# Performance work log

Measured on AMD Instinct MI355X. Metric: run time of the kernel, lower is better.

The kernel has to match this reference:

```python
import jax, jax.numpy as jnp
import numpy as np

B, N, C, D, H = 2, 1024, 64, 512, 16
HD = D // H
LENGTH_SCALE = 0.22
LN_EPS = 1e-5


def _ln(x, g, b):
    m = jnp.mean(x, axis=-1, keepdims=True)
    v = jnp.var(x, axis=-1, keepdims=True)
    return g * (x - m) * jax.lax.rsqrt(v + LN_EPS) + b


def _distance_affinity(positions, length_scale):
    # Gaussian affinity in [0,1]: exp(-||pi - pj||^2 / (2 ls^2))
    d2 = jnp.sum((positions[:, :, None, :] - positions[:, None, :, :]) ** 2, axis=-1)
    return jnp.exp(-d2 / (2.0 * length_scale * length_scale))


def setup_inputs() -> dict:
    key = jax.random.key(0)
    ks = jax.random.split(key, 24)
    p = lambda k, s: (jax.random.normal(k, s) * 0.02).astype(jnp.float32)
    hidden = jax.random.normal(ks[0], (B, N, D), jnp.float32)
    adjacency = (jax.random.uniform(ks[1], (B, N, N)) < 0.05).astype(jnp.float32)
    positions = jax.random.uniform(ks[2], (B, N, 2), jnp.float32)
    context_tokens = jax.random.normal(ks[3], (B, C, D), jnp.float32)
    edge_head_conditioning = (jax.random.normal(ks[4], (B, 4, N, N)) * 0.1).astype(jnp.float32)
    return {
        'hidden': hidden, 'adjacency': adjacency, 'positions': positions,
        'context_tokens': context_tokens, 'edge_head_conditioning': edge_head_conditioning,
        'Wq': p(ks[5], (D, D)), 'bq': jnp.zeros((D,), jnp.float32),
        'Wk': p(ks[6], (D, D)), 'bk': jnp.zeros((D,), jnp.float32),
        'Wv': p(ks[7], (D, D)), 'bv': jnp.zeros((D,), jnp.float32),
        'Wo': p(ks[8], (D, D)), 'bo': jnp.zeros((D,), jnp.float32),
        'ln1_g': jnp.ones((D,), jnp.float32), 'ln1_b': jnp.zeros((D,), jnp.float32),
        'ln2_g': jnp.ones((D,), jnp.float32), 'ln2_b': jnp.zeros((D,), jnp.float32),
        'W1': p(ks[9], (4 * D, D)), 'b1': jnp.zeros((4 * D,), jnp.float32),
        'W2': p(ks[10], (D, 4 * D)), 'b2': jnp.zeros((D,), jnp.float32),
    }


def _forward(hidden, adjacency, positions, context_tokens, edge_head_conditioning,
             Wq, bq, Wk, bk, Wv, bv, Wo, bo, ln1_g, ln1_b, ln2_g, ln2_b, W1, b1, W2, b2):
    b, n, d = hidden.shape
    cc = context_tokens.shape[1]
    hd = d // H
    n1 = _ln(hidden, ln1_g, ln1_b)
    nc = _ln(context_tokens, ln1_g, ln1_b)
    key_source = jnp.concatenate([n1, nc], axis=1)          # [b, m, d]
    m = n + cc
    q = (n1 @ Wq.T + bq).reshape(b, n, H, hd).transpose(0, 2, 1, 3)          # [b,h,n,hd]
    k = (key_source @ Wk.T + bk).reshape(b, m, H, hd).transpose(0, 2, 1, 3)  # [b,h,m,hd]
    v = (key_source @ Wv.T + bv).reshape(b, m, H, hd).transpose(0, 2, 1, 3)
    logits = jnp.einsum('bhnd,bhmd->bhnm', q, k) / jnp.sqrt(jnp.float32(hd))

    pad = jnp.zeros((b, n, cc), logits.dtype)
    dist_e = jnp.concatenate([_distance_affinity(positions, LENGTH_SCALE), pad], axis=-1)  # [b,n,m]
    adj_e = jnp.concatenate([adjacency, pad], axis=-1)                                      # [b,n,m]
    edge_e = jnp.concatenate([edge_head_conditioning,
                              jnp.zeros((b, 4, n, cc), logits.dtype)], axis=-1)             # [b,4,n,m]

    # heads 0:4 distance, 4:8 connectivity, 8:12 stress (edge cond), 12:16 free
    bias = jnp.concatenate([
        jnp.broadcast_to((2.0 * dist_e - 1.0)[:, None], (b, 4, n, m)),
        jnp.broadcast_to((2.0 * adj_e - 1.0)[:, None], (b, 4, n, m)),
        edge_e,
        jnp.zeros((b, 4, n, m), logits.dtype)], axis=1)
    scale = jnp.concatenate([
        jnp.broadcast_to((0.25 + 0.75 * dist_e)[:, None], (b, 4, n, m)),
        jnp.broadcast_to((0.25 + 0.75 * adj_e)[:, None], (b, 4, n, m)),
        jnp.ones((b, 8, n, m), logits.dtype)], axis=1)

    w = jax.nn.softmax(logits + bias, axis=-1) * scale
    w = w / jnp.maximum(jnp.sum(w, axis=-1, keepdims=True), 1e-6)
    att = jnp.einsum('bhnm,bhmd->bhnd', w, v).transpose(0, 2, 1, 3).reshape(b, n, d)
    hidden = hidden + att @ Wo.T + bo
    n2 = _ln(hidden, ln2_g, ln2_b)
    ff = jax.nn.gelu(n2 @ W1.T + b1, approximate=False) @ W2.T + b2
    return hidden + ff


def reference(hidden, adjacency, positions, context_tokens, edge_head_conditioning,
              Wq, bq, Wk, bk, Wv, bv, Wo, bo, ln1_g, ln1_b, ln2_g, ln2_b, W1, b1, W2, b2):
    return _forward(hidden, adjacency, positions, context_tokens, edge_head_conditioning,
                    Wq, bq, Wk, bk, Wv, bv, Wo, bo, ln1_g, ln1_b, ln2_g, ln2_b, W1, b1, W2, b2)
```

## Files before the change

### kernel.cpp

```cpp
#include <hip/hip_runtime.h>
#include <math.h>

typedef unsigned short u16;
typedef unsigned int u32;
typedef __attribute__((ext_vector_type(8))) short short8;
typedef __attribute__((ext_vector_type(8))) u16 ushort8_t;
typedef __attribute__((ext_vector_type(4))) u16 ushort4_t;
typedef __attribute__((ext_vector_type(4))) float floatx4;

#define DEV static __device__ __forceinline__

DEV u16 f2b(float f) {
    union { float f; u32 u; } v; v.f = f;
    u32 u = v.u;
    return (u16)((u + 0x7fffu + ((u >> 16) & 1u)) >> 16);
}
DEV float gelu_f(float x) {
    return 0.5f * x * (1.f + erff(x * 0.70710678118654752f));
}

__global__ __launch_bounds__(256) void cvt_weights(
    const float* __restrict__ wq, const float* __restrict__ wk,
    const float* __restrict__ wv, const float* __restrict__ wo,
    const float* __restrict__ w1, const float* __restrict__ w2,
    u16* __restrict__ oq, u16* __restrict__ ok, u16* __restrict__ ov,
    u16* __restrict__ oo, u16* __restrict__ o1, u16* __restrict__ o2)
{
    long i = ((long)blockIdx.x * 256 + threadIdx.x) * 4;
    const float* s; u16* d; long off;
    if (i < 1048576) {
        int seg = (int)(i >> 18);
        off = i & 262143;
        s = seg == 0 ? wq : seg == 1 ? wk : seg == 2 ? wv : wo;
        d = seg == 0 ? oq : seg == 1 ? ok : seg == 2 ? ov : oo;
    } else if (i < 2097152) {
        off = i - 1048576; s = w1; d = o1;
    } else {
        off = i - 2097152; s = w2; d = o2;
    }
    floatx4 v = *(const floatx4*)(s + off);
    ushort4_t r;
    r[0] = f2b(v[0]); r[1] = f2b(v[1]); r[2] = f2b(v[2]); r[3] = f2b(v[3]);
    *(ushort4_t*)(d + off) = r;
}

__global__ __launch_bounds__(256) void ln_kernel(
    const float* __restrict__ hidden, const float* __restrict__ ctx,
    const float* __restrict__ g, const float* __restrict__ bta,
    u16* __restrict__ dst, int nrows)
{
    int wid = threadIdx.x >> 6, lane = threadIdx.x & 63;
    int row = blockIdx.x * 4 + wid;
    if (row >= nrows) return;
    int bi = row / 1088, loc = row % 1088;
    const float* src = (loc < 1024) ? hidden + ((long)(bi * 1024 + loc)) * 512
                                    : ctx + ((long)(bi * 64 + (loc - 1024))) * 512;
    const floatx4* p = (const floatx4*)(src + lane * 8);
    floatx4 a = p[0], b4 = p[1];
    float x[8];
    x[0] = a[0]; x[1] = a[1]; x[2] = a[2]; x[3] = a[3];
    x[4] = b4[0]; x[5] = b4[1]; x[6] = b4[2]; x[7] = b4[3];
    float s = 0.f, sq = 0.f;
#pragma unroll
    for (int j = 0; j < 8; j++) { s += x[j]; sq += x[j] * x[j]; }
#pragma unroll
    for (int m = 1; m < 64; m <<= 1) {
        s += __shfl_xor(s, m, 64);
        sq += __shfl_xor(sq, m, 64);
    }
    float mean = s * (1.f / 512.f);
    float var = sq * (1.f / 512.f) - mean * mean;
    float rstd = rsqrtf(var + 1e-5f);
    const floatx4* gp = (const floatx4*)(g + lane * 8);
    const floatx4* bp = (const floatx4*)(bta + lane * 8);
    floatx4 g0 = gp[0], g1 = gp[1], bb0 = bp[0], bb1 = bp[1];
    float gg[8], bbv[8];
    gg[0] = g0[0]; gg[1] = g0[1]; gg[2] = g0[2]; gg[3] = g0[3];
    gg[4] = g1[0]; gg[5] = g1[1]; gg[6] = g1[2]; gg[7] = g1[3];
    bbv[0] = bb0[0]; bbv[1] = bb0[1]; bbv[2] = bb0[2]; bbv[3] = bb0[3];
    bbv[4] = bb1[0]; bbv[5] = bb1[1]; bbv[6] = bb1[2]; bbv[7] = bb1[3];
    ushort8_t o;
#pragma unroll
    for (int j = 0; j < 8; j++) o[j] = f2b((x[j] - mean) * rstd * gg[j] + bbv[j]);
    *(ushort8_t*)(dst + (long)row * 512 + lane * 8) = o;
}

template<int ACT, int OMODE>
__global__ __launch_bounds__(256) void gemm_bt(
    const u16* __restrict__ A, const u16* __restrict__ Bw,
    const float* __restrict__ bias0, const float* __restrict__ bias1,
    const float* __restrict__ bias2,
    float* __restrict__ outf, u16* __restrict__ outb0,
    u16* __restrict__ outb1, u16* __restrict__ outb2,
    int M, int N, int K, int ksp)
{
    __shared__ u16 As[128 * 72];
    __shared__ u16 Bs[128 * 72];
    int tid = threadIdx.x;
    int wid = tid >> 6, lane = tid & 63;
    int l16 = lane & 15, lq = lane >> 4;
    int m0 = blockIdx.y * 128, n0 = blockIdx.x * 128;
    int wm = (wid >> 1) * 64, wn = (wid & 1) * 64;
    int srow = tid >> 3;
    int scol = (tid & 7) * 8;
    int kb0 = (OMODE == 4) ? blockIdx.z * ksp : 0;
    int kend = (OMODE == 4) ? kb0 + ksp : K;
    floatx4 acc[4][4] = {};
    for (int k0 = kb0; k0 < kend; k0 += 64) {
#pragma unroll
        for (int p = 0; p < 4; p++) {
            int r = p * 32 + srow;
            *(ushort8_t*)(As + r * 72 + scol) =
                *(const ushort8_t*)(A + (long)(m0 + r) * K + k0 + scol);
            *(ushort8_t*)(Bs + r * 72 + scol) =
                *(const ushort8_t*)(Bw + (long)(n0 + r) * K + k0 + scol);
        }
        __syncthreads();
#pragma unroll
        for (int s = 0; s < 2; s++) {
            short8 af[4], bfr[4];
#pragma unroll
            for (int i = 0; i < 4; i++)
                af[i] = *(const short8*)(As + (wm + i * 16 + l16) * 72 + s * 32 + lq * 8);
#pragma unroll
            for (int j = 0; j < 4; j++)
                bfr[j] = *(const short8*)(Bs + (wn + j * 16 + l16) * 72 + s * 32 + lq * 8);
#pragma unroll
            for (int i = 0; i < 4; i++)
#pragma unroll
                for (int j = 0; j < 4; j++)
                    acc[i][j] = __builtin_amdgcn_mfma_f32_16x16x32_bf16(
                        af[i], bfr[j], acc[i][j], 0, 0, 0);
        }
        __syncthreads();
    }
#pragma unroll
    for (int i = 0; i < 4; i++) {
#pragma unroll
        for (int j = 0; j < 4; j++) {
            int gmb = m0 + wm + i * 16 + lq * 4;
            int gn = n0 + wn + j * 16 + l16;
#pragma unroll
            for (int r = 0; r < 4; r++) {
                int gm = gmb + r;
                float v = acc[i][j][r];
                if (OMODE == 1) {
                    v += bias0[gn];
                    if (ACT == 1) v = gelu_f(v);
                    outb0[(long)gm * N + gn] = f2b(v);
                } else if (OMODE == 3) {
                    if (gn < 512) {
                        outb0[(long)gm * 512 + gn] = f2b(v + bias0[gn]);
                    } else if (gn < 1024) {
                        outb1[(long)gm * 512 + gn - 512] = f2b(v + bias1[gn - 512]);
                    } else {
                        int bi = gm / 1088, tok = gm % 1088;
                        int col = gn - 1024;
                        outb2[((long)((bi * 16 + (col >> 5)) * 32 + (col & 31))) * 1088 + tok]
                            = f2b(v + bias2[col]);
                    }
                } else {
                    outf[((long)blockIdx.z * M + gm) * N + gn] = v;
                }
            }
        }
    }
}

__global__ __launch_bounds__(256) void attn_kernel(
    const u16* __restrict__ qb, const u16* __restrict__ kb,
    const u16* __restrict__ vt, const float* __restrict__ adj,
    const float* __restrict__ pos, const float* __restrict__ ehc,
    float* __restrict__ o_part, float* __restrict__ l_part)
{
    __shared__ u16 P[4][16 * 72];
    __shared__ float ubuf[4][1088];
    int b = blockIdx.z >> 1, split = blockIdx.z & 1;
    int h = blockIdx.y, grp = h >> 2;
    int qbase = blockIdx.x * 64;
    int tid = threadIdx.x, wid = tid >> 6, lane = tid & 63;
    int l16 = lane & 15, lq = lane >> 4;
    int kv_begin = split ? 576 : 0;
    int kv_end = split ? 1088 : 576;
    const float inv2ls2 = 10.330578512396695f;
    const float rs = 0.17677669529663687f;
    float* pls = &ubuf[0][0];
    float* bt = ubuf[wid];

    if (grp == 0) {
        for (int t = tid; t < 2048; t += 256) pls[t] = pos[b * 2048 + t];
        __syncthreads();
    }
    int rowbase = qbase + wid * 16;
    int qrow = rowbase + l16;
    short8 qa = *(const short8*)(qb + ((long)(b * 1088 + qrow)) * 512 + h * 32 + lq * 8);
    int irow[4];
#pragma unroll
    for (int r = 0; r < 4; r++) irow[r] = rowbase + lq * 4 + r;
    float ipx[4], ipy[4];
    if (grp == 0) {
#pragma unroll
        for (int r = 0; r < 4; r++) {
            ipx[r] = pls[irow[r] * 2];
            ipy[r] = pls[irow[r] * 2 + 1];
        }
    }

    bool stg = (grp == 1 || grp == 2);
    const float* src = (grp == 1)
        ? adj + ((long)(b * 1024 + rowbase)) * 1024
        : ehc + (((long)(b * 4 + (h - 8))) * 1024 + rowbase) * 1024;
    int row4 = lane >> 4, c16 = (lane & 15) * 4;
    floatx4 pre[4];

    float rsum[4] = {0.f, 0.f, 0.f, 0.f};
    floatx4 o[2] = {};
    floatx4 zacc = {0.f, 0.f, 0.f, 0.f};
    u16* Pw = P[wid];

    if (stg && kv_begin < 1024) {
#pragma unroll
        for (int p = 0; p < 4; p++)
            pre[p] = *(const floatx4*)(src + (long)(p * 4 + row4) * 1024 + kv_begin + c16);
#pragma unroll
        for (int p = 0; p < 4; p++)
            *(floatx4*)(bt + (p * 4 + row4) * 68 + c16) = pre[p];
    }

    for (int kv = kv_begin; kv < kv_end; kv += 64) {
        floatx4 sfr[4];
#pragma unroll
        for (int jf = 0; jf < 4; jf++) {
            int tok = kv + jf * 16 + l16;
            short8 kf = *(const short8*)(kb + ((long)(b * 1088 + tok)) * 512 + h * 32 + lq * 8);
            sfr[jf] = __builtin_amdgcn_mfma_f32_16x16x32_bf16(qa, kf, zacc, 0, 0, 0);
        }
        int kvn = kv + 64;
        bool pf = stg && kvn < kv_end && kvn < 1024;
        if (pf) {
#pragma unroll
            for (int p = 0; p < 4; p++)
                pre[p] = *(const floatx4*)(src + (long)(p * 4 + row4) * 1024 + kvn + c16);
        }
#pragma unroll
        for (int jf = 0; jf < 4; jf++) {
            int j = kv + jf * 16 + l16;
            float px = 0.f, py = 0.f;
            if (grp == 0 && j < 1024) { px = pls[2 * j]; py = pls[2 * j + 1]; }
#pragma unroll
            for (int r = 0; r < 4; r++) {
                float bias, scale;
                if (grp == 0) {
                    if (j < 1024) {
                        float dx = ipx[r] - px, dy = ipy[r] - py;
                        float e = __expf(-(dx * dx + dy * dy) * inv2ls2);
                        bias = 2.f * e - 1.f; scale = 0.25f + 0.75f * e;
                    } else { bias = -1.f; scale = 0.25f; }
                } else if (grp == 1) {
                    if (j < 1024) {
                        float a = bt[(lq * 4 + r) * 68 + jf * 16 + l16];
                        bias = 2.f * a - 1.f; scale = 0.25f + 0.75f * a;
                    } else { bias = -1.f; scale = 0.25f; }
                } else if (grp == 2) {
                    bias = (j < 1024) ? bt[(lq * 4 + r) * 68 + jf * 16 + l16] : 0.f;
                    scale = 1.f;
                } else { bias = 0.f; scale = 1.f; }
                float sv = fminf(sfr[jf][r] * rs + bias, 60.f);
                float p = __expf(sv) * scale;
                rsum[r] += p;
                Pw[(lq * 4 + r) * 72 + jf * 16 + l16] = f2b(p);
            }
        }
#pragma unroll
        for (int s = 0; s < 2; s++) {
            short8 pa = *(const short8*)(Pw + l16 * 72 + s * 32 + lq * 8);
#pragma unroll
            for (int nf = 0; nf < 2; nf++) {
                const u16* vrow = vt + ((long)((b * 16 + h) * 32 + nf * 16 + l16)) * 1088
                                  + kv + s * 32 + lq * 8;
                short8 vf = *(const short8*)vrow;
                o[nf] = __builtin_amdgcn_mfma_f32_16x16x32_bf16(pa, vf, o[nf], 0, 0, 0);
            }
        }
        if (pf) {
#pragma unroll
            for (int p = 0; p < 4; p++)
                *(floatx4*)(bt + (p * 4 + row4) * 68 + c16) = pre[p];
        }
    }
#pragma unroll
    for (int r = 0; r < 4; r++) {
#pragma unroll
        for (int m = 1; m < 16; m <<= 1)
            rsum[r] += __shfl_xor(rsum[r], m, 64);
    }
    long pb = (((long)(split * 2 + b) * 16 + h) * 1024);
#pragma unroll
    for (int nf = 0; nf < 2; nf++)
#pragma unroll
        for (int r = 0; r < 4; r++)
            o_part[(pb + irow[r]) * 32 + nf * 16 + l16] = o[nf][r];
    if (l16 == 0) {
#pragma unroll
        for (int r = 0; r < 4; r++) l_part[pb + irow[r]] = rsum[r];
    }
}

__global__ __launch_bounds__(256) void attn_combine(
    const float* __restrict__ o_part, const float* __restrict__ l_part,
    u16* __restrict__ att)
{
    int idx = blockIdx.x * 256 + threadIdx.x;
    int c4 = idx & 7;
    int row = (idx >> 3) & 1023;
    int h = (idx >> 13) & 15;
    int b = (idx >> 17) & 1;
    long base = (((long)b * 16 + h) * 1024 + row) * 32 + c4 * 4;
    floatx4 a0 = *(const floatx4*)(o_part + base);
    floatx4 a1 = *(const floatx4*)(o_part + 1048576 + base);
    long lb0 = ((long)b * 16 + h) * 1024 + row;
    float inv = 1.f / (l_part[lb0] + l_part[32768 + lb0]);
    ushort4_t w;
#pragma unroll
    for (int e = 0; e < 4; e++) w[e] = f2b((a0[e] + a1[e]) * inv);
    *(ushort4_t*)(att + ((long)b * 1024 + row) * 512 + h * 32 + c4 * 4) = w;
}

__global__ __launch_bounds__(256) void wo_ln2(
    const float* __restrict__ p0, const float* __restrict__ p1,
    const float* __restrict__ bo, const float* __restrict__ hidden,
    const float* __restrict__ g, const float* __restrict__ bta,
    float* __restrict__ h2, u16* __restrict__ n2)
{
    int wid = threadIdx.x >> 6, lane = threadIdx.x & 63;
    int row = blockIdx.x * 4 + wid;
    long base = (long)row * 512 + lane * 8;
    float x[8];
#pragma unroll
    for (int hp = 0; hp < 2; hp++) {
        floatx4 a = *(const floatx4*)(hidden + base + hp * 4);
        floatx4 q0 = *(const floatx4*)(p0 + base + hp * 4);
        floatx4 q1 = *(const floatx4*)(p1 + base + hp * 4);
        floatx4 bb = *(const floatx4*)(bo + lane * 8 + hp * 4);
#pragma unroll
        for (int e = 0; e < 4; e++) x[hp * 4 + e] = a[e] + q0[e] + q1[e] + bb[e];
    }
    float s = 0.f, sq = 0.f;
#pragma unroll
    for (int j = 0; j < 8; j++) { s += x[j]; sq += x[j] * x[j]; }
#pragma unroll
    for (int m = 1; m < 64; m <<= 1) {
        s += __shfl_xor(s, m, 64);
        sq += __shfl_xor(sq, m, 64);
    }
    float mean = s * (1.f / 512.f);
    float var = sq * (1.f / 512.f) - mean * mean;
    float rstd = rsqrtf(var + 1e-5f);
#pragma unroll
    for (int hp = 0; hp < 2; hp++) {
        floatx4 w;
#pragma unroll
        for (int e = 0; e < 4; e++) w[e] = x[hp * 4 + e];
        *(floatx4*)(h2 + base + hp * 4) = w;
    }
    const floatx4* gp = (const floatx4*)(g + lane * 8);
    const floatx4* bp = (const floatx4*)(bta + lane * 8);
    floatx4 g0 = gp[0], g1 = gp[1], bb0 = bp[0], bb1 = bp[1];
    float gg[8], bbv[8];
    gg[0] = g0[0]; gg[1] = g0[1]; gg[2] = g0[2]; gg[3] = g0[3];
    gg[4] = g1[0]; gg[5] = g1[1]; gg[6] = g1[2]; gg[7] = g1[3];
    bbv[0] = bb0[0]; bbv[1] = bb0[1]; bbv[2] = bb0[2]; bbv[3] = bb0[3];
    bbv[4] = bb1[0]; bbv[5] = bb1[1]; bbv[6] = bb1[2]; bbv[7] = bb1[3];
    ushort8_t ov;
#pragma unroll
    for (int j = 0; j < 8; j++) ov[j] = f2b((x[j] - mean) * rstd * gg[j] + bbv[j]);
    *(ushort8_t*)(n2 + base) = ov;
}

__global__ __launch_bounds__(256) void ff2_ep(
    const float* __restrict__ parts, const float* __restrict__ b2,
    const float* __restrict__ h2, float* __restrict__ out)
{
    long idx = ((long)blockIdx.x * 256 + threadIdx.x) * 4;
    int col = (int)(idx & 511);
    floatx4 v = *(const floatx4*)(h2 + idx);
    floatx4 bb = *(const floatx4*)(b2 + col);
#pragma unroll
    for (int s = 0; s < 4; s++) {
        floatx4 p = *(const floatx4*)(parts + (long)s * 1048576 + idx);
#pragma unroll
        for (int e = 0; e < 4; e++) v[e] += p[e];
    }
#pragma unroll
    for (int e = 0; e < 4; e++) v[e] += bb[e];
    *(floatx4*)(out + idx) = v;
}

extern "C" void kernel_launch(void* const* d_in, const int* in_sizes, int n_in,
                              void* d_out, int out_size, void* d_ws, size_t ws_size,
                              hipStream_t stream) {
    const float* hidden = (const float*)d_in[0];
    const float* adjacency = (const float*)d_in[1];
    const float* positions = (const float*)d_in[2];
    const float* context = (const float*)d_in[3];
    const float* ehc = (const float*)d_in[4];
    const float* Wq = (const float*)d_in[5];
    const float* bq = (const float*)d_in[6];
    const float* Wk = (const float*)d_in[7];
    const float* bk = (const float*)d_in[8];
    const float* Wv = (const float*)d_in[9];
    const float* bv = (const float*)d_in[10];
    const float* Wo = (const float*)d_in[11];
    const float* bo = (const float*)d_in[12];
    const float* ln1g = (const float*)d_in[13];
    const float* ln1b = (const float*)d_in[14];
    const float* ln2g = (const float*)d_in[15];
    const float* ln2b = (const float*)d_in[16];
    const float* W1 = (const float*)d_in[17];
    const float* b1 = (const float*)d_in[18];
    const float* W2 = (const float*)d_in[19];
    const float* b2 = (const float*)d_in[20];
    float* out = (float*)d_out;

    char* ws = (char*)d_ws;
    u16* wqkv_b = (u16*)(ws + 0);
    u16* wo_b   = (u16*)(ws + 1572864);
    u16* w1_b   = (u16*)(ws + 2097152);
    u16* w2_b   = (u16*)(ws + 4194304);
    u16* ks_b   = (u16*)(ws + 6291456);
    u16* q_b    = (u16*)(ws + 8519680);
    u16* k_b    = (u16*)(ws + 10747904);
    u16* vt_b   = (u16*)(ws + 12976128);
    u16* att_b  = (u16*)(ws + 15204352);
    float* h2_f = (float*)(ws + 17301504);
    u16* n2_b   = (u16*)(ws + 21495808);
    u16* g_b    = (u16*)(ws + 23592960);
    float* o_part = (float*)(ws + 31981568);
    float* l_part = (float*)(ws + 40370176);
    float* wo_p  = (float*)(ws + 40632320);
    float* ff2_p = (float*)(ws + 49020928);

    cvt_weights<<<3072, 256, 0, stream>>>(Wq, Wk, Wv, Wo, W1, W2,
                                          wqkv_b, wqkv_b + 262144, wqkv_b + 524288,
                                          wo_b, w1_b, w2_b);
    ln_kernel<<<544, 256, 0, stream>>>(hidden, context, ln1g, ln1b, ks_b, 2176);
    gemm_bt<0, 3><<<dim3(12, 17), 256, 0, stream>>>(
        ks_b, wqkv_b, bq, bk, bv, nullptr, q_b, k_b, vt_b, 2176, 1536, 512, 0);
    attn_kernel<<<dim3(16, 16, 4), 256, 0, stream>>>(
        q_b, k_b, vt_b, adjacency, positions, ehc, o_part, l_part);
    attn_combine<<<1024, 256, 0, stream>>>(o_part, l_part, att_b);
    gemm_bt<0, 4><<<dim3(4, 16, 2), 256, 0, stream>>>(
        att_b, wo_b, nullptr, nullptr, nullptr, wo_p, nullptr, nullptr, nullptr,
        2048, 512, 512, 256);
    wo_ln2<<<512, 256, 0, stream>>>(wo_p, wo_p + 1048576, bo, hidden,
                                    ln2g, ln2b, h2_f, n2_b);
    gemm_bt<1, 1><<<dim3(16, 16), 256, 0, stream>>>(
        n2_b, w1_b, b1, nullptr, nullptr, nullptr, g_b, nullptr, nullptr,
        2048, 2048, 512, 0);
    gemm_bt<0, 4><<<dim3(4, 16, 4), 256, 0, stream>>>(
        g_b, w2_b, nullptr, nullptr, nullptr, ff2_p, nullptr, nullptr, nullptr,
        2048, 512, 2048, 512);
    ff2_ep<<<1024, 256, 0, stream>>>(ff2_p, b2, h2_f, out);
}
```

Before: 246.8 us.

## Fuse prep kernels, prefetch GEMM tiles, split attention four ways, atomic FF2 epilogue

Merges weight conversion and LN1 into one launch. The GEMM tile shrinks to 64x128 and next-tile global loads are register-prefetched behind the MFMA work. Attention KV is split four ways instead of two, the bias tile is stored in bf16 LDS, the q scaling is folded into the QKV epilogue, and the kernel gets an occupancy hint. The final FF2 GEMM atomically accumulates into the output, which wo_ln2 pre-initialises with residual plus b2, so the separate epilogue kernel is dropped. The cost is extra atomics and a bf16 rounding of the bias values.

```diff
diff --git a/kernel.cpp b/kernel.cpp
--- a/kernel.cpp
+++ b/kernel.cpp
@@ -15,43 +15,46 @@
     u32 u = v.u;
     return (u16)((u + 0x7fffu + ((u >> 16) & 1u)) >> 16);
 }
+DEV float b2f(u16 h) {
+    union { u32 u; float f; } v; v.u = ((u32)h) << 16;
+    return v.f;
+}
 DEV float gelu_f(float x) {
     return 0.5f * x * (1.f + erff(x * 0.70710678118654752f));
 }
 
-__global__ __launch_bounds__(256) void cvt_weights(
+__global__ __launch_bounds__(256) void cvt_ln(
     const float* __restrict__ wq, const float* __restrict__ wk,
     const float* __restrict__ wv, const float* __restrict__ wo,
     const float* __restrict__ w1, const float* __restrict__ w2,
     u16* __restrict__ oq, u16* __restrict__ ok, u16* __restrict__ ov,
-    u16* __restrict__ oo, u16* __restrict__ o1, u16* __restrict__ o2)
-{
-    long i = ((long)blockIdx.x * 256 + threadIdx.x) * 4;
-    const float* s; u16* d; long off;
-    if (i < 1048576) {
-        int seg = (int)(i >> 18);
-        off = i & 262143;
-        s = seg == 0 ? wq : seg == 1 ? wk : seg == 2 ? wv : wo;
-        d = seg == 0 ? oq : seg == 1 ? ok : seg == 2 ? ov : oo;
-    } else if (i < 2097152) {
-        off = i - 1048576; s = w1; d = o1;
-    } else {
-        off = i - 2097152; s = w2; d = o2;
-    }
-    floatx4 v = *(const floatx4*)(s + off);
-    ushort4_t r;
-    r[0] = f2b(v[0]); r[1] = f2b(v[1]); r[2] = f2b(v[2]); r[3] = f2b(v[3]);
-    *(ushort4_t*)(d + off) = r;
-}
-
-__global__ __launch_bounds__(256) void ln_kernel(
+    u16* __restrict__ oo, u16* __restrict__ o1, u16* __restrict__ o2,
     const float* __restrict__ hidden, const float* __restrict__ ctx,
     const float* __restrict__ g, const float* __restrict__ bta,
-    u16* __restrict__ dst, int nrows)
+    u16* __restrict__ dst)
 {
+    if (blockIdx.x < 3072) {
+        long i = ((long)blockIdx.x * 256 + threadIdx.x) * 4;
+        const float* s; u16* d; long off;
+        if (i < 1048576) {
+            int seg = (int)(i >> 18);
+            off = i & 262143;
+            s = seg == 0 ? wq : seg == 1 ? wk : seg == 2 ? wv : wo;
+            d = seg == 0 ? oq : seg == 1 ? ok : seg == 2 ? ov : oo;
+        } else if (i < 2097152) {
+            off = i - 1048576; s = w1; d = o1;
+        } else {
+            off = i - 2097152; s = w2; d = o2;
+        }
+        floatx4 v = *(const floatx4*)(s + off);
+        ushort4_t r;
+        r[0] = f2b(v[0]); r[1] = f2b(v[1]); r[2] = f2b(v[2]); r[3] = f2b(v[3]);
+        *(ushort4_t*)(d + off) = r;
+        return;
+    }
     int wid = threadIdx.x >> 6, lane = threadIdx.x & 63;
-    int row = blockIdx.x * 4 + wid;
-    if (row >= nrows) return;
+    int row = (blockIdx.x - 3072) * 4 + wid;
+    if (row >= 2176) return;
     int bi = row / 1088, loc = row % 1088;
     const float* src = (loc < 1024) ? hidden + ((long)(bi * 1024 + loc)) * 512
                                     : ctx + ((long)(bi * 64 + (loc - 1024))) * 512;
@@ -94,39 +97,55 @@
     u16* __restrict__ outb1, u16* __restrict__ outb2,
     int M, int N, int K, int ksp)
 {
-    __shared__ u16 As[128 * 72];
+    __shared__ u16 As[64 * 72];
     __shared__ u16 Bs[128 * 72];
     int tid = threadIdx.x;
     int wid = tid >> 6, lane = tid & 63;
     int l16 = lane & 15, lq = lane >> 4;
-    int m0 = blockIdx.y * 128, n0 = blockIdx.x * 128;
-    int wm = (wid >> 1) * 64, wn = (wid & 1) * 64;
+    int m0 = blockIdx.y * 64, n0 = blockIdx.x * 128;
+    int wm = (wid >> 1) * 32, wn = (wid & 1) * 64;
     int srow = tid >> 3;
     int scol = (tid & 7) * 8;
-    int kb0 = (OMODE == 4) ? blockIdx.z * ksp : 0;
-    int kend = (OMODE == 4) ? kb0 + ksp : K;
-    floatx4 acc[4][4] = {};
+    int kb0 = (OMODE >= 4) ? blockIdx.z * ksp : 0;
+    int kend = (OMODE >= 4) ? kb0 + ksp : K;
+    floatx4 acc[2][4] = {};
+    const u16* Ap = A + (long)(m0 + srow) * K + scol;
+    const u16* Bp = Bw + (long)(n0 + srow) * K + scol;
+    ushort8_t pa[2], pb[4];
+#pragma unroll
+    for (int p = 0; p < 2; p++)
+        pa[p] = *(const ushort8_t*)(Ap + (long)p * 32 * K + kb0);
+#pragma unroll
+    for (int p = 0; p < 4; p++)
+        pb[p] = *(const ushort8_t*)(Bp + (long)p * 32 * K + kb0);
     for (int k0 = kb0; k0 < kend; k0 += 64) {
 #pragma unroll
-        for (int p = 0; p < 4; p++) {
-            int r = p * 32 + srow;
-            *(ushort8_t*)(As + r * 72 + scol) =
-                *(const ushort8_t*)(A + (long)(m0 + r) * K + k0 + scol);
-            *(ushort8_t*)(Bs + r * 72 + scol) =
-                *(const ushort8_t*)(Bw + (long)(n0 + r) * K + k0 + scol);
-        }
+        for (int p = 0; p < 2; p++)
+            *(ushort8_t*)(As + (p * 32 + srow) * 72 + scol) = pa[p];
+#pragma unroll
+        for (int p = 0; p < 4; p++)
+            *(ushort8_t*)(Bs + (p * 32 + srow) * 72 + scol) = pb[p];
         __syncthreads();
+        int k1 = k0 + 64;
+        if (k1 < kend) {
+#pragma unroll
+            for (int p = 0; p < 2; p++)
+                pa[p] = *(const ushort8_t*)(Ap + (long)p * 32 * K + k1);
+#pragma unroll
+            for (int p = 0; p < 4; p++)
+                pb[p] = *(const ushort8_t*)(Bp + (long)p * 32 * K + k1);
+        }
 #pragma unroll
         for (int s = 0; s < 2; s++) {
-            short8 af[4], bfr[4];
-#pragma unroll
-            for (int i = 0; i < 4; i++)
+            short8 af[2], bfr[4];
+#pragma unroll
+            for (int i = 0; i < 2; i++)
                 af[i] = *(const short8*)(As + (wm + i * 16 + l16) * 72 + s * 32 + lq * 8);
 #pragma unroll
             for (int j = 0; j < 4; j++)
                 bfr[j] = *(const short8*)(Bs + (wn + j * 16 + l16) * 72 + s * 32 + lq * 8);
 #pragma unroll
-            for (int i = 0; i < 4; i++)
+            for (int i = 0; i < 2; i++)
 #pragma unroll
                 for (int j = 0; j < 4; j++)
                     acc[i][j] = __builtin_amdgcn_mfma_f32_16x16x32_bf16(
@@ -134,8 +153,9 @@
         }
         __syncthreads();
     }
-#pragma unroll
-    for (int i = 0; i < 4; i++) {
+    const float rs = 0.17677669529663687f;
+#pragma unroll
+    for (int i = 0; i < 2; i++) {
 #pragma unroll
         for (int j = 0; j < 4; j++) {
             int gmb = m0 + wm + i * 16 + lq * 4;
@@ -150,7 +170,7 @@
                     outb0[(long)gm * N + gn] = f2b(v);
                 } else if (OMODE == 3) {
                     if (gn < 512) {
-                        outb0[(long)gm * 512 + gn] = f2b(v + bias0[gn]);
+                        outb0[(long)gm * 512 + gn] = f2b((v + bias0[gn]) * rs);
                     } else if (gn < 1024) {
                         outb1[(long)gm * 512 + gn - 512] = f2b(v + bias1[gn - 512]);
                     } else {
@@ -159,33 +179,34 @@
                         outb2[((long)((bi * 16 + (col >> 5)) * 32 + (col & 31))) * 1088 + tok]
                             = f2b(v + bias2[col]);
                     }
+                } else if (OMODE == 4) {
+                    outf[((long)blockIdx.z * M + gm) * N + gn] = v;
                 } else {
-                    outf[((long)blockIdx.z * M + gm) * N + gn] = v;
+                    atomicAdd(outf + (long)gm * N + gn, v);
                 }
             }
         }
     }
 }
 
-__global__ __launch_bounds__(256) void attn_kernel(
+__global__ __launch_bounds__(256, 6) void attn_kernel(
     const u16* __restrict__ qb, const u16* __restrict__ kb,
     const u16* __restrict__ vt, const float* __restrict__ adj,
     const float* __restrict__ pos, const float* __restrict__ ehc,
     float* __restrict__ o_part, float* __restrict__ l_part)
 {
-    __shared__ u16 P[4][16 * 72];
-    __shared__ float ubuf[4][1088];
-    int b = blockIdx.z >> 1, split = blockIdx.z & 1;
+    __shared__ u16 P[4][1152];
+    __shared__ u16 ub[4][1152];
+    int b = blockIdx.z >> 2, split = blockIdx.z & 3;
     int h = blockIdx.y, grp = h >> 2;
     int qbase = blockIdx.x * 64;
     int tid = threadIdx.x, wid = tid >> 6, lane = tid & 63;
     int l16 = lane & 15, lq = lane >> 4;
-    int kv_begin = split ? 576 : 0;
-    int kv_end = split ? 1088 : 576;
+    int kv_begin = (split == 0) ? 0 : 320 + (split - 1) * 256;
+    int kv_end = (split == 3) ? 1088 : 320 + split * 256;
     const float inv2ls2 = 10.330578512396695f;
-    const float rs = 0.17677669529663687f;
-    float* pls = &ubuf[0][0];
-    float* bt = ubuf[wid];
+    float* pls = (float*)&ub[0][0];
+    u16* bt = ub[wid];
 
     if (grp == 0) {
         for (int t = tid; t < 2048; t += 256) pls[t] = pos[b * 2048 + t];
@@ -223,8 +244,12 @@
         for (int p = 0; p < 4; p++)
             pre[p] = *(const floatx4*)(src + (long)(p * 4 + row4) * 1024 + kv_begin + c16);
 #pragma unroll
-        for (int p = 0; p < 4; p++)
-            *(floatx4*)(bt + (p * 4 + row4) * 68 + c16) = pre[p];
+        for (int p = 0; p < 4; p++) {
+            ushort4_t w4;
+#pragma unroll
+            for (int e = 0; e < 4; e++) w4[e] = f2b(pre[p][e]);
+            *(ushort4_t*)(bt + (p * 4 + row4) * 72 + c16) = w4;
+        }
     }
 
     for (int kv = kv_begin; kv < kv_end; kv += 64) {
@@ -258,14 +283,14 @@
                     } else { bias = -1.f; scale = 0.25f; }
                 } else if (grp == 1) {
                     if (j < 1024) {
-                        float a = bt[(lq * 4 + r) * 68 + jf * 16 + l16];
+                        float a = b2f(bt[(lq * 4 + r) * 72 + jf * 16 + l16]);
                         bias = 2.f * a - 1.f; scale = 0.25f + 0.75f * a;
                     } else { bias = -1.f; scale = 0.25f; }
                 } else if (grp == 2) {
-                    bias = (j < 1024) ? bt[(lq * 4 + r) * 68 + jf * 16 + l16] : 0.f;
+                    bias = (j < 1024) ? b2f(bt[(lq * 4 + r) * 72 + jf * 16 + l16]) : 0.f;
                     scale = 1.f;
                 } else { bias = 0.f; scale = 1.f; }
-                float sv = fminf(sfr[jf][r] * rs + bias, 60.f);
+                float sv = fminf(sfr[jf][r] + bias, 60.f);
                 float p = __expf(sv) * scale;
                 rsum[r] += p;
                 Pw[(lq * 4 + r) * 72 + jf * 16 + l16] = f2b(p);
@@ -284,8 +309,12 @@
         }
         if (pf) {
 #pragma unroll
-            for (int p = 0; p < 4; p++)
-                *(floatx4*)(bt + (p * 4 + row4) * 68 + c16) = pre[p];
+            for (int p = 0; p < 4; p++) {
+                ushort4_t w4;
+#pragma unroll
+                for (int e = 0; e < 4; e++) w4[e] = f2b(pre[p][e]);
+                *(ushort4_t*)(bt + (p * 4 + row4) * 72 + c16) = w4;
+            }
         }
     }
 #pragma unroll
@@ -316,13 +345,20 @@
     int h = (idx >> 13) & 15;
     int b = (idx >> 17) & 1;
     long base = (((long)b * 16 + h) * 1024 + row) * 32 + c4 * 4;
-    floatx4 a0 = *(const floatx4*)(o_part + base);
-    floatx4 a1 = *(const floatx4*)(o_part + 1048576 + base);
     long lb0 = ((long)b * 16 + h) * 1024 + row;
-    float inv = 1.f / (l_part[lb0] + l_part[32768 + lb0]);
+    floatx4 a = {0.f, 0.f, 0.f, 0.f};
+    float lsum = 0.f;
+#pragma unroll
+    for (int s = 0; s < 4; s++) {
+        floatx4 p = *(const floatx4*)(o_part + (long)s * 1048576 + base);
+#pragma unroll
+        for (int e = 0; e < 4; e++) a[e] += p[e];
+        lsum += l_part[(long)s * 32768 + lb0];
+    }
+    float inv = 1.f / lsum;
     ushort4_t w;
 #pragma unroll
-    for (int e = 0; e < 4; e++) w[e] = f2b((a0[e] + a1[e]) * inv);
+    for (int e = 0; e < 4; e++) w[e] = f2b(a[e] * inv);
     *(ushort4_t*)(att + ((long)b * 1024 + row) * 512 + h * 32 + c4 * 4) = w;
 }
 
@@ -330,7 +366,8 @@
     const float* __restrict__ p0, const float* __restrict__ p1,
     const float* __restrict__ bo, const float* __restrict__ hidden,
     const float* __restrict__ g, const float* __restrict__ bta,
-    float* __restrict__ h2, u16* __restrict__ n2)
+    const float* __restrict__ b2, float* __restrict__ out,
+    u16* __restrict__ n2)
 {
     int wid = threadIdx.x >> 6, lane = threadIdx.x & 63;
     int row = blockIdx.x * 4 + wid;
@@ -358,10 +395,11 @@
     float rstd = rsqrtf(var + 1e-5f);
 #pragma unroll
     for (int hp = 0; hp < 2; hp++) {
+        floatx4 bb2 = *(const floatx4*)(b2 + lane * 8 + hp * 4);
         floatx4 w;
 #pragma unroll
-        for (int e = 0; e < 4; e++) w[e] = x[hp * 4 + e];
-        *(floatx4*)(h2 + base + hp * 4) = w;
+        for (int e = 0; e < 4; e++) w[e] = x[hp * 4 + e] + bb2[e];
+        *(floatx4*)(out + base + hp * 4) = w;
     }
     const floatx4* gp = (const floatx4*)(g + lane * 8);
     const floatx4* bp = (const floatx4*)(bta + lane * 8);
@@ -375,25 +413,6 @@
 #pragma unroll
     for (int j = 0; j < 8; j++) ov[j] = f2b((x[j] - mean) * rstd * gg[j] + bbv[j]);
     *(ushort8_t*)(n2 + base) = ov;
-}
-
-__global__ __launch_bounds__(256) void ff2_ep(
-    const float* __restrict__ parts, const float* __restrict__ b2,
-    const float* __restrict__ h2, float* __restrict__ out)
-{
-    long idx = ((long)blockIdx.x * 256 + threadIdx.x) * 4;
-    int col = (int)(idx & 511);
-    floatx4 v = *(const floatx4*)(h2 + idx);
-    floatx4 bb = *(const floatx4*)(b2 + col);
-#pragma unroll
-    for (int s = 0; s < 4; s++) {
-        floatx4 p = *(const floatx4*)(parts + (long)s * 1048576 + idx);
-#pragma unroll
-        for (int e = 0; e < 4; e++) v[e] += p[e];
-    }
-#pragma unroll
-    for (int e = 0; e < 4; e++) v[e] += bb[e];
-    *(floatx4*)(out + idx) = v;
 }
 
 extern "C" void kernel_launch(void* const* d_in, const int* in_sizes, int n_in,
@@ -432,33 +451,30 @@
     u16* k_b    = (u16*)(ws + 10747904);
     u16* vt_b   = (u16*)(ws + 12976128);
     u16* att_b  = (u16*)(ws + 15204352);
-    float* h2_f = (float*)(ws + 17301504);
-    u16* n2_b   = (u16*)(ws + 21495808);
-    u16* g_b    = (u16*)(ws + 23592960);
-    float* o_part = (float*)(ws + 31981568);
-    float* l_part = (float*)(ws + 40370176);
-    float* wo_p  = (float*)(ws + 40632320);
-    float* ff2_p = (float*)(ws + 49020928);
-
-    cvt_weights<<<3072, 256, 0, stream>>>(Wq, Wk, Wv, Wo, W1, W2,
-                                          wqkv_b, wqkv_b + 262144, wqkv_b + 524288,
-                                          wo_b, w1_b, w2_b);
-    ln_kernel<<<544, 256, 0, stream>>>(hidden, context, ln1g, ln1b, ks_b, 2176);
-    gemm_bt<0, 3><<<dim3(12, 17), 256, 0, stream>>>(
+    u16* n2_b   = (u16*)(ws + 17301504);
+    u16* g_b    = (u16*)(ws + 19398656);
+    float* o_part = (float*)(ws + 27787264);
+    float* l_part = (float*)(ws + 44564480);
+    float* wo_p  = (float*)(ws + 45088768);
+
+    cvt_ln<<<3616, 256, 0, stream>>>(Wq, Wk, Wv, Wo, W1, W2,
+                                     wqkv_b, wqkv_b + 262144, wqkv_b + 524288,
+                                     wo_b, w1_b, w2_b,
+                                     hidden, context, ln1g, ln1b, ks_b);
+    gemm_bt<0, 3><<<dim3(12, 34), 256, 0, stream>>>(
         ks_b, wqkv_b, bq, bk, bv, nullptr, q_b, k_b, vt_b, 2176, 1536, 512, 0);
-    attn_kernel<<<dim3(16, 16, 4), 256, 0, stream>>>(
+    attn_kernel<<<dim3(16, 16, 8), 256, 0, stream>>>(
         q_b, k_b, vt_b, adjacency, positions, ehc, o_part, l_part);
     attn_combine<<<1024, 256, 0, stream>>>(o_part, l_part, att_b);
-    gemm_bt<0, 4><<<dim3(4, 16, 2), 256, 0, stream>>>(
+    gemm_bt<0, 4><<<dim3(4, 32, 2), 256, 0, stream>>>(
         att_b, wo_b, nullptr, nullptr, nullptr, wo_p, nullptr, nullptr, nullptr,
         2048, 512, 512, 256);
     wo_ln2<<<512, 256, 0, stream>>>(wo_p, wo_p + 1048576, bo, hidden,
-                                    ln2g, ln2b, h2_f, n2_b);
-    gemm_bt<1, 1><<<dim3(16, 16), 256, 0, stream>>>(
+                                    ln2g, ln2b, b2, out, n2_b);
+    gemm_bt<1, 1><<<dim3(16, 32), 256, 0, stream>>>(
         n2_b, w1_b, b1, nullptr, nullptr, nullptr, g_b, nullptr, nullptr,
         2048, 2048, 512, 0);
-    gemm_bt<0, 4><<<dim3(4, 16, 4), 256, 0, stream>>>(
-        g_b, w2_b, nullptr, nullptr, nullptr, ff2_p, nullptr, nullptr, nullptr,
+    gemm_bt<0, 5><<<dim3(4, 32, 4), 256, 0, stream>>>(
+        g_b, w2_b, nullptr, nullptr, nullptr, out, nullptr, nullptr, nullptr,
         2048, 512, 2048, 512);
-    ff2_ep<<<1024, 256, 0, stream>>>(ff2_p, b2, h2_f, out);
-}
+}
```

Result: slower. 265.0 us (+7.4%).
